# Optimization experiments

Measured on AMD Instinct MI355X. Metric: run time of the kernel, lower is better.

## Reference

```python
import jax, jax.numpy as jnp
import numpy as np

B, NQ, NK = 8, 1024, 1024
DQ = DK = DV = 512
H = 8
DS = DV // H
EPS = 1e-4
MAX_ITER = 3
SQRT_V = DV ** 0.25  # sqrt(sqrt(dim_V))


def setup_inputs() -> dict:
    key = jax.random.key(0)
    ks = jax.random.split(key, 8)
    s = 0.02
    return {
        "Q": jax.random.normal(ks[0], (B, NQ, DQ), jnp.float32),
        "K": jax.random.normal(ks[1], (B, NK, DK), jnp.float32),
        "Wq": jax.random.normal(ks[2], (DV, DQ), jnp.float32) * s,
        "bq": jnp.zeros((DV,), jnp.float32),
        "Wk": jax.random.normal(ks[3], (DV, DK), jnp.float32) * s,
        "bk": jnp.zeros((DV,), jnp.float32),
        "Wv": jax.random.normal(ks[4], (DV, DK), jnp.float32) * s,
        "bv": jnp.zeros((DV,), jnp.float32),
        "Wo": jax.random.normal(ks[5], (DV, DV), jnp.float32) * s,
        "bo": jnp.zeros((DV,), jnp.float32),
    }


def _split_heads(x):
    # torch.cat(x.split(ds, 2), 0): head-major stacking along batch
    b, n, _ = x.shape
    return x.reshape(b, n, H, DS).transpose(2, 0, 1, 3).reshape(H * b, n, DS)


def _merge_heads(x, b):
    # torch.cat(x.split(b, 0), 2): inverse of _split_heads
    _, n, ds = x.shape
    return x.reshape(H, b, n, ds).transpose(1, 2, 0, 3).reshape(b, n, H * ds)


def _sinkhorn_plan(x, y):
    # x: [M, P1, d], y: [M, P2, d]; cost = pairwise Euclidean (p=2) distance.
    x2 = jnp.sum(x * x, axis=-1)[:, :, None]
    y2 = jnp.sum(y * y, axis=-1)[:, None, :]
    C = jnp.sqrt(jnp.maximum(x2 + y2 - 2.0 * jnp.einsum("mid,mjd->mij", x, y), 0.0))
    m, p1, p2 = C.shape
    log_a = -jnp.log(jnp.float32(p1))  # uniform marginals
    log_b = -jnp.log(jnp.float32(p2))
    u = jnp.zeros((m, p1), C.dtype)
    v = jnp.zeros((m, p2), C.dtype)
    for _ in range(MAX_ITER):  # fixed small iteration count (max_iter=3)
        u = EPS * (log_a - jax.scipy.special.logsumexp((v[:, None, :] - C) / EPS, axis=2))
        v = EPS * (log_b - jax.scipy.special.logsumexp((u[:, :, None] - C) / EPS, axis=1))
    # transport plan P: [M, P1, P2]
    return jnp.exp((u[:, :, None] + v[:, None, :] - C) / EPS)


def reference(Q, K, Wq, bq, Wk, bk, Wv, bv, Wo, bo):
    q = Q @ Wq.T + bq            # [B, NQ, DV]
    k = K @ Wk.T + bk            # [B, NK, DV]
    v = K @ Wv.T + bv            # [B, NK, DV]
    b = Q.shape[0]
    q_, k_, v_ = _split_heads(q), _split_heads(k), _split_heads(v)  # [H*B, N, DS]
    A = _sinkhorn_plan(q_ / SQRT_V, k_ / SQRT_V)                    # [H*B, NQ, NK]
    O = _merge_heads(q_ + jnp.einsum("mij,mjd->mid", A, v_), b)     # [B, NQ, DV]
    return O + jax.nn.relu(O @ Wo.T + bo)
```

## Files before the change

kernel.cpp:

```cpp
#include <hip/hip_runtime.h>
#include <hip/hip_bf16.h>
#include <math.h>

#define NB 8
#define NN 1024
#define ND 512
#define NH 8
#define NDS 64
#define NM 64
#define LOG_A (-6.93147180559945f)
#define SQRT_V 4.75682846001088f
#define INV_SQRT_V 0.210224103813429f
#define INV_EPS 10000.0f
#define L2E  1.44269504088896f
#define LN2F 0.693147180559945f
#define IEL2 14426.9504088896f

#define SPLIT_ELEMS ((size_t)NM * NN * NDS)
#define W_ELEMS     ((size_t)ND * ND)
#define UV_FLOATS   ((size_t)NM * NN)

typedef unsigned short u16;
typedef unsigned int   u32;
typedef __attribute__((ext_vector_type(8))) short bf16x8;
typedef __attribute__((ext_vector_type(4))) float f32x4;

#define MFMA16(a,b,c) __builtin_amdgcn_mfma_f32_16x16x32_bf16(a,b,c,0,0,0)

__device__ __forceinline__ u16 f2bf_t(float x) {
  return (u16)(__float_as_uint(x) >> 16);
}
__device__ __forceinline__ float bf2f(u16 h) {
  return __uint_as_float(((u32)h) << 16);
}
__device__ __forceinline__ float fast_sqrt(float x) {
  float r;
  asm("v_sqrt_f32 %0, %1" : "=v"(r) : "v"(x));
  return r;
}
__device__ __forceinline__ float fast_exp2(float x) {
  float r;
  asm("v_exp_f32 %0, %1" : "=v"(r) : "v"(x));
  return r;
}
__device__ __forceinline__ float max3f(float a, float b, float c) {
  float r;
  asm("v_max3_f32 %0, %1, %2, %3" : "=v"(r) : "v"(a), "v"(b), "v"(c));
  return r;
}
__device__ __forceinline__ void soft_barrier() {
  asm volatile("s_waitcnt lgkmcnt(0)" ::: "memory");
  __builtin_amdgcn_sched_barrier(0);
  __builtin_amdgcn_s_barrier();
  __builtin_amdgcn_sched_barrier(0);
  asm volatile("" ::: "memory");
}

__global__ __launch_bounds__(256) void k_split(
    const float* __restrict__ X, u16* __restrict__ hi, u16* __restrict__ lo)
{
  const size_t i = ((size_t)blockIdx.x * 256 + threadIdx.x) * 4;
  float4 v = *(const float4*)&X[i];
  const float* vp = (const float*)&v;
  u16 h[4], l[4];
#pragma unroll
  for (int j = 0; j < 4; ++j) {
    h[j] = f2bf_t(vp[j]);
    l[j] = f2bf_t(vp[j] - bf2f(h[j]));
  }
  uint2 ph, pl;
  ph.x = (u32)h[0] | ((u32)h[1] << 16);
  ph.y = (u32)h[2] | ((u32)h[3] << 16);
  pl.x = (u32)l[0] | ((u32)l[1] << 16);
  pl.y = (u32)l[2] | ((u32)l[3] << 16);
  *(uint2*)&hi[i] = ph;
  *(uint2*)&lo[i] = pl;
}

__global__ __launch_bounds__(256, 2) void k_proj_mfma(
    const u16* __restrict__ Xh, const u16* __restrict__ Xl,
    const u16* __restrict__ Wh, const u16* __restrict__ Wl,
    const float* __restrict__ bias, u16* __restrict__ oh,
    u16* __restrict__ ol, u16* __restrict__ oT,
    float* __restrict__ nrm, float scale, int mode)
{
  __shared__ __align__(16) u16 Xhs[2][64][72];
  __shared__ __align__(16) u16 Xls[2][64][72];
  __shared__ __align__(16) u16 Whs[2][64][72];
  __shared__ __align__(16) u16 Wls[2][64][72];
  const int t = threadIdx.x;
  const int r0 = blockIdx.x * 64;
  const int h  = blockIdx.y;
  const int c0 = h * 64;
  const int w = t >> 6, l = t & 63;
  const int c = l & 15, kg = l >> 4;
  const int srow = t >> 2;
  const int skoff = (t & 3) * 16;

  const u16* gxh = &Xh[(size_t)(r0 + srow) * ND + skoff];
  const u16* gxl = &Xl[(size_t)(r0 + srow) * ND + skoff];
  const u16* gwh = &Wh[(size_t)(c0 + srow) * ND + skoff];
  const u16* gwl = &Wl[(size_t)(c0 + srow) * ND + skoff];

  bf16x8 rxh0 = *(const bf16x8*)gxh, rxh1 = *(const bf16x8*)(gxh + 8);
  bf16x8 rxl0 = *(const bf16x8*)gxl, rxl1 = *(const bf16x8*)(gxl + 8);
  bf16x8 rwh0 = *(const bf16x8*)gwh, rwh1 = *(const bf16x8*)(gwh + 8);
  bf16x8 rwl0 = *(const bf16x8*)gwl, rwl1 = *(const bf16x8*)(gwl + 8);

  f32x4 acc[4];
#pragma unroll
  for (int cf = 0; cf < 4; ++cf) acc[cf] = (f32x4){0.f, 0.f, 0.f, 0.f};

  for (int kt = 0; kt < 8; ++kt) {
    const int buf = kt & 1;
    *(bf16x8*)&Xhs[buf][srow][skoff]     = rxh0;
    *(bf16x8*)&Xhs[buf][srow][skoff + 8] = rxh1;
    *(bf16x8*)&Xls[buf][srow][skoff]     = rxl0;
    *(bf16x8*)&Xls[buf][srow][skoff + 8] = rxl1;
    *(bf16x8*)&Whs[buf][srow][skoff]     = rwh0;
    *(bf16x8*)&Whs[buf][srow][skoff + 8] = rwh1;
    *(bf16x8*)&Wls[buf][srow][skoff]     = rwl0;
    *(bf16x8*)&Wls[buf][srow][skoff + 8] = rwl1;
    {
      const int nk = ((kt + 1) & 7) * 64;
      rxh0 = *(const bf16x8*)(gxh + nk); rxh1 = *(const bf16x8*)(gxh + nk + 8);
      rxl0 = *(const bf16x8*)(gxl + nk); rxl1 = *(const bf16x8*)(gxl + nk + 8);
      rwh0 = *(const bf16x8*)(gwh + nk); rwh1 = *(const bf16x8*)(gwh + nk + 8);
      rwl0 = *(const bf16x8*)(gwl + nk); rwl1 = *(const bf16x8*)(gwl + nk + 8);
    }
    soft_barrier();
#pragma unroll
    for (int ks = 0; ks < 2; ++ks) {
      bf16x8 Ah = *(const bf16x8*)&Xhs[buf][w * 16 + c][ks * 32 + kg * 8];
      bf16x8 Al = *(const bf16x8*)&Xls[buf][w * 16 + c][ks * 32 + kg * 8];
#pragma unroll
      for (int cf = 0; cf < 4; ++cf) {
        bf16x8 Bh = *(const bf16x8*)&Whs[buf][cf * 16 + c][ks * 32 + kg * 8];
        bf16x8 Bl = *(const bf16x8*)&Wls[buf][cf * 16 + c][ks * 32 + kg * 8];
        acc[cf] = MFMA16(Ah, Bh, acc[cf]);
        acc[cf] = MFMA16(Ah, Bl, acc[cf]);
        acc[cf] = MFMA16(Al, Bh, acc[cf]);
      }
    }
  }

  const int bb = r0 >> 10;
  const int n0 = r0 & 1023;
  const size_t mrow = (size_t)(h * NB + bb) * NN;
  if (mode == 0) {
    float ns[4] = {0.f, 0.f, 0.f, 0.f};
#pragma unroll
    for (int cf = 0; cf < 4; ++cf) {
      const int col = c0 + cf * 16 + c;
      const float bv = bias[col];
#pragma unroll
      for (int r = 0; r < 4; ++r) {
        float v = (acc[cf][r] + bv) * scale;
        u16 hv = f2bf_t(v);
        u16 lv = f2bf_t(v - bf2f(hv));
        ns[r] = fmaf(v, v, ns[r]);
        int n = n0 + w * 16 + kg * 4 + r;
        size_t idx = (mrow + n) * NDS + cf * 16 + c;
        oh[idx] = hv;
        ol[idx] = lv;
      }
    }
#pragma unroll
    for (int off = 1; off <= 8; off <<= 1)
#pragma unroll
      for (int r = 0; r < 4; ++r) ns[r] += __shfl_xor(ns[r], off);
    if (c == 0) {
#pragma unroll
      for (int r = 0; r < 4; ++r)
        nrm[mrow + n0 + w * 16 + kg * 4 + r] = ns[r];
    }
  } else {
#pragma unroll
    for (int cf = 0; cf < 4; ++cf) {
      const int d = cf * 16 + c;
      const float bv = bias[c0 + d];
      u16 p0 = f2bf_t((acc[cf][0] + bv) * scale);
      u16 p1 = f2bf_t((acc[cf][1] + bv) * scale);
      u16 p2 = f2bf_t((acc[cf][2] + bv) * scale);
      u16 p3 = f2bf_t((acc[cf][3] + bv) * scale);
      uint2 p;
      p.x = (u32)p0 | ((u32)p1 << 16);
      p.y = (u32)p2 | ((u32)p3 << 16);
      *(uint2*)&oT[((size_t)(h * NB + bb) * NDS + d) * NN + n0 + w * 16 + kg * 4] = p;
    }
  }
}

__global__ __launch_bounds__(512, 4) void k_lse_mfma(
    const u16* __restrict__ Ah_, const u16* __restrict__ Bh_,
    const float* __restrict__ Anrm, const float* __restrict__ Bnrm,
    const float* __restrict__ din, float* __restrict__ dout, int first)
{
  __shared__ __align__(16) float din_s[NN];
  __shared__ __align__(16) float y2_s[NN];
  __shared__ __align__(16) u16 Bhs[2][64][72];
  const int t = threadIdx.x;
  const int Lb = blockIdx.x;
  const int xcd = Lb & 7, slot = Lb >> 3;
  const int m = xcd + 8 * (slot >> 3);
  const int a0 = (slot & 7) * 128;

  if (first) {
    *(float2*)&din_s[t * 2] = make_float2(0.f, 0.f);
  } else {
    float2 dv = *(const float2*)&din[(size_t)m * NN + t * 2];
    dv.x *= L2E; dv.y *= L2E;
    *(float2*)&din_s[t * 2] = dv;
  }
  *(float2*)&y2_s[t * 2] = *(const float2*)&Bnrm[(size_t)m * NN + t * 2];

  const int w = t >> 6, l = t & 63;
  const int c = l & 15, kg = l >> 4;
  const int arow = a0 + w * 16;
  const size_t mbase = (size_t)m * NN * NDS;

  const u16* pah = &Ah_[mbase + (size_t)(arow + c) * NDS + kg * 8];
  bf16x8 A0h = *(const bf16x8*)pah;
  bf16x8 A1h = *(const bf16x8*)(pah + 32);

  float x2r[4];
#pragma unroll
  for (int r = 0; r < 4; ++r) x2r[r] = Anrm[(size_t)m * NN + arow + kg * 4 + r];
  float M[4], S[4];
#pragma unroll
  for (int r = 0; r < 4; ++r) { M[r] = -3.0e38f; S[r] = 0.f; }

  const int srow = t >> 3;
  const int skoff = (t & 7) * 8;
  const u16* gh = &Bh_[mbase + (size_t)srow * NDS + skoff];
  bf16x8 rh = *(const bf16x8*)gh;
  __syncthreads();

  for (int bt = 0; bt < 16; ++bt) {
    const int b0 = bt * 64;
    const int buf = bt & 1;
    *(bf16x8*)&Bhs[buf][srow][skoff] = rh;
    {
      const size_t noff = (size_t)((bt + 1) & 15) * 4096;
      rh = *(const bf16x8*)(gh + noff);
    }
    soft_barrier();
    f32x4 acc[4];
#pragma unroll
    for (int cf = 0; cf < 4; ++cf) {
      const int bl = cf * 16 + c;
      bf16x8 B0h = *(const bf16x8*)&Bhs[buf][bl][kg * 8];
      bf16x8 B1h = *(const bf16x8*)&Bhs[buf][bl][kg * 8 + 32];
      f32x4 a = {0.f, 0.f, 0.f, 0.f};
      a = MFMA16(A0h, B0h, a);
      a = MFMA16(A1h, B1h, a);
      acc[cf] = a;
    }
    float X[4][4];
#pragma unroll
    for (int cf = 0; cf < 4; ++cf) {
      const int col = b0 + cf * 16 + c;
      const float vb2 = din_s[col];
      const float y2  = y2_s[col];
#pragma unroll
      for (int r = 0; r < 4; ++r) {
        float d2 = fmaf(-2.f, acc[cf][r], x2r[r] + y2);
        float sq = fast_sqrt(fmaxf(d2, 0.f));
        X[cf][r] = fmaf(-IEL2, sq, vb2);
      }
    }
#pragma unroll
    for (int r = 0; r < 4; ++r) {
      float m1 = max3f(X[0][r], X[1][r], X[2][r]);
      float nm = max3f(m1, X[3][r], M[r]);
      float s4 = fast_exp2(X[0][r] - nm) + fast_exp2(X[1][r] - nm)
               + fast_exp2(X[2][r] - nm) + fast_exp2(X[3][r] - nm);
      S[r] = fmaf(S[r], fast_exp2(M[r] - nm), s4);
      M[r] = nm;
    }
  }
#pragma unroll
  for (int off = 1; off <= 8; off <<= 1) {
#pragma unroll
    for (int r = 0; r < 4; ++r) {
      float Mo = __shfl_xor(M[r], off);
      float So = __shfl_xor(S[r], off);
      float nm = fmaxf(M[r], Mo);
      S[r] = S[r] * fast_exp2(M[r] - nm) + So * fast_exp2(Mo - nm);
      M[r] = nm;
    }
  }
  if (c == 0) {
#pragma unroll
    for (int r = 0; r < 4; ++r)
      dout[(size_t)m * NN + arow + kg * 4 + r] =
          LOG_A - M[r] * LN2F - __logf(S[r]);
  }
}

__global__ __launch_bounds__(512, 4) void k_pv_mfma(
    const u16* __restrict__ qh, const u16* __restrict__ ql,
    const u16* __restrict__ kh, const u16* __restrict__ vT,
    const float* __restrict__ qn, const float* __restrict__ kn,
    const float* __restrict__ ue, const float* __restrict__ ve,
    u16* __restrict__ Oh_, u16* __restrict__ Ol_)
{
  __shared__ __align__(16) float ve_s[NN];
  __shared__ __align__(16) float y2_s[NN];
  __shared__ __align__(16) u16 Bhs[2][64][72];
  __shared__ __align__(16) u16 Vs[2][64][72];
  __shared__ __align__(16) u16 pT[8][16][40];
  const int t = threadIdx.x;
  const int Lb = blockIdx.x;
  const int xcd = Lb & 7, slot = Lb >> 3;
  const int m = xcd + 8 * (slot >> 3);
  const int a0 = (slot & 7) * 128;
  {
    float2 vv = *(const float2*)&ve[(size_t)m * NN + t * 2];
    vv.x *= L2E; vv.y *= L2E;
    *(float2*)&ve_s[t * 2] = vv;
  }
  *(float2*)&y2_s[t * 2] = *(const float2*)&kn[(size_t)m * NN + t * 2];

  const int w = t >> 6, l = t & 63;
  const int c = l & 15, kg = l >> 4;
  const int arow = a0 + w * 16;
  const size_t mbase = (size_t)m * NN * NDS;

  const u16* pah = &qh[mbase + (size_t)(arow + c) * NDS + kg * 8];
  bf16x8 A0h = *(const bf16x8*)pah;
  bf16x8 A1h = *(const bf16x8*)(pah + 32);

  float x2r[4], uer2[4];
#pragma unroll
  for (int r = 0; r < 4; ++r) {
    x2r[r]  = qn[(size_t)m * NN + arow + kg * 4 + r];
    uer2[r] = ue[(size_t)m * NN + arow + kg * 4 + r] * L2E;
  }
  f32x4 pacc[4];
#pragma unroll
  for (int df = 0; df < 4; ++df) pacc[df] = (f32x4){0.f, 0.f, 0.f, 0.f};

  const int srow = t >> 3;
  const int skoff = (t & 7) * 8;
  const u16* gh = &kh[mbase + (size_t)srow * NDS + skoff];
  const u16* gv = &vT[((size_t)m * NDS + srow) * NN + skoff];
  bf16x8 rh = *(const bf16x8*)gh;
  bf16x8 rv = *(const bf16x8*)gv;
  __syncthreads();

  for (int bt = 0; bt < 16; ++bt) {
    const int b0 = bt * 64;
    const int buf = bt & 1;
    *(bf16x8*)&Bhs[buf][srow][skoff] = rh;
    *(bf16x8*)&Vs[buf][srow][skoff]  = rv;
    {
      const int nbt = (bt + 1) & 15;
      rh = *(const bf16x8*)(gh + (size_t)nbt * 4096);
      rv = *(const bf16x8*)(gv + (size_t)nbt * 64);
    }
    soft_barrier();
#pragma unroll
    for (int ph = 0; ph < 2; ++ph) {
      f32x4 acc[2];
#pragma unroll
      for (int q = 0; q < 2; ++q) {
        const int cf = ph * 2 + q;
        const int bl = cf * 16 + c;
        bf16x8 B0h = *(const bf16x8*)&Bhs[buf][bl][kg * 8];
        bf16x8 B1h = *(const bf16x8*)&Bhs[buf][bl][kg * 8 + 32];
        f32x4 a = {0.f, 0.f, 0.f, 0.f};
        a = MFMA16(A0h, B0h, a);
        a = MFMA16(A1h, B1h, a);
        acc[q] = a;
      }
#pragma unroll
      for (int q = 0; q < 2; ++q) {
        const int cf = ph * 2 + q;
        const int col = b0 + cf * 16 + c;
        const float ve2 = ve_s[col];
        const float y2  = y2_s[col];
#pragma unroll
        for (int r = 0; r < 4; ++r) {
          float d2 = fmaf(-2.f, acc[q][r], x2r[r] + y2);
          float sq = fast_sqrt(fmaxf(d2, 0.f));
          float p  = fast_exp2(fmaf(-IEL2, sq, uer2[r] + ve2));
          pT[w][kg * 4 + r][q * 16 + c] = f2bf_t(p);
        }
      }
      bf16x8 Pa = *(const bf16x8*)&pT[w][c][kg * 8];
#pragma unroll
      for (int df = 0; df < 4; ++df) {
        bf16x8 Vb = *(const bf16x8*)&Vs[buf][df * 16 + c][ph * 32 + kg * 8];
        pacc[df] = MFMA16(Pa, Vb, pacc[df]);
      }
    }
  }
#pragma unroll
  for (int df = 0; df < 4; ++df) {
#pragma unroll
    for (int r = 0; r < 4; ++r) {
      int row = arow + kg * 4 + r;
      int d = df * 16 + c;
      size_t qi = mbase + (size_t)row * NDS + d;
      float qv = bf2f(qh[qi]) + bf2f(ql[qi]);
      float o  = fmaf(SQRT_V, qv, pacc[df][r]);
      u16 hv = f2bf_t(o);
      Oh_[qi] = hv;
      Ol_[qi] = f2bf_t(o - bf2f(hv));
    }
  }
}

__global__ __launch_bounds__(256, 2) void k_out_mfma(
    const u16* __restrict__ Oh_, const u16* __restrict__ Ol_,
    const u16* __restrict__ Wh, const u16* __restrict__ Wl,
    const float* __restrict__ bo, float* __restrict__ out)
{
  __shared__ __align__(16) u16 Ahs[2][64][72];
  __shared__ __align__(16) u16 Als[2][64][72];
  __shared__ __align__(16) u16 Whs[2][64][72];
  __shared__ __align__(16) u16 Wls[2][64][72];
  const int t = threadIdx.x;
  const int r0 = blockIdx.x * 64;
  const int c0 = blockIdx.y * 64;
  const int bb = r0 >> 10;
  const int n0 = r0 & 1023;
  const int w = t >> 6, l = t & 63;
  const int c = l & 15, kg = l >> 4;
  const int srow = t >> 2;
  const int skoff = (t & 3) * 16;

  f32x4 acc[4];
#pragma unroll
  for (int cf = 0; cf < 4; ++cf) acc[cf] = (f32x4){0.f, 0.f, 0.f, 0.f};

  bf16x8 rah0, rah1, ral0, ral1, rwh0, rwh1, rwl0, rwl1;
  {
    const size_t ob = ((size_t)(0 * NB + bb) * NN + n0 + srow) * NDS;
    const u16* gah = &Oh_[ob + skoff];
    const u16* gal = &Ol_[ob + skoff];
    const u16* gwh = &Wh[(size_t)(c0 + srow) * ND + skoff];
    const u16* gwl = &Wl[(size_t)(c0 + srow) * ND + skoff];
    rah0 = *(const bf16x8*)gah; rah1 = *(const bf16x8*)(gah + 8);
    ral0 = *(const bf16x8*)gal; ral1 = *(const bf16x8*)(gal + 8);
    rwh0 = *(const bf16x8*)gwh; rwh1 = *(const bf16x8*)(gwh + 8);
    rwl0 = *(const bf16x8*)gwl; rwl1 = *(const bf16x8*)(gwl + 8);
  }

  for (int kt = 0; kt < 8; ++kt) {
    const int buf = kt & 1;
    *(bf16x8*)&Ahs[buf][srow][skoff]     = rah0;
    *(bf16x8*)&Ahs[buf][srow][skoff + 8] = rah1;
    *(bf16x8*)&Als[buf][srow][skoff]     = ral0;
    *(bf16x8*)&Als[buf][srow][skoff + 8] = ral1;
    *(bf16x8*)&Whs[buf][srow][skoff]     = rwh0;
    *(bf16x8*)&Whs[buf][srow][skoff + 8] = rwh1;
    *(bf16x8*)&Wls[buf][srow][skoff]     = rwl0;
    *(bf16x8*)&Wls[buf][srow][skoff + 8] = rwl1;
    {
      const int nkt = (kt + 1) & 7;
      const size_t ob = ((size_t)(nkt * NB + bb) * NN + n0 + srow) * NDS;
      const u16* gah = &Oh_[ob + skoff];
      const u16* gal = &Ol_[ob + skoff];
      const u16* gwh = &Wh[(size_t)(c0 + srow) * ND + nkt * 64 + skoff];
      const u16* gwl = &Wl[(size_t)(c0 + srow) * ND + nkt * 64 + skoff];
      rah0 = *(const bf16x8*)gah; rah1 = *(const bf16x8*)(gah + 8);
      ral0 = *(const bf16x8*)gal; ral1 = *(const bf16x8*)(gal + 8);
      rwh0 = *(const bf16x8*)gwh; rwh1 = *(const bf16x8*)(gwh + 8);
      rwl0 = *(const bf16x8*)gwl; rwl1 = *(const bf16x8*)(gwl + 8);
    }
    soft_barrier();
#pragma unroll
    for (int ks = 0; ks < 2; ++ks) {
      bf16x8 Ah = *(const bf16x8*)&Ahs[buf][w * 16 + c][ks * 32 + kg * 8];
      bf16x8 Al = *(const bf16x8*)&Als[buf][w * 16 + c][ks * 32 + kg * 8];
#pragma unroll
      for (int cf = 0; cf < 4; ++cf) {
        bf16x8 Bh = *(const bf16x8*)&Whs[buf][cf * 16 + c][ks * 32 + kg * 8];
        bf16x8 Bl = *(const bf16x8*)&Wls[buf][cf * 16 + c][ks * 32 + kg * 8];
        acc[cf] = MFMA16(Ah, Bh, acc[cf]);
        acc[cf] = MFMA16(Ah, Bl, acc[cf]);
        acc[cf] = MFMA16(Al, Bh, acc[cf]);
      }
    }
  }
#pragma unroll
  for (int cf = 0; cf < 4; ++cf) {
    const int col = c0 + cf * 16 + c;
    const int d = cf * 16 + c;
    const float bv = bo[col];
#pragma unroll
    for (int r = 0; r < 4; ++r) {
      const int n = n0 + w * 16 + kg * 4 + r;
      const size_t oi = ((size_t)(blockIdx.y * NB + bb) * NN + n) * NDS + d;
      float om = bf2f(Oh_[oi]) + bf2f(Ol_[oi]);
      out[(size_t)(r0 + w * 16 + kg * 4 + r) * ND + col] =
          om + fmaxf(acc[cf][r] + bv, 0.f);
    }
  }
}

extern "C" void kernel_launch(void* const* d_in, const int* in_sizes, int n_in,
                              void* d_out, int out_size, void* d_ws, size_t ws_size,
                              hipStream_t stream) {
  const float* Q  = (const float*)d_in[0];
  const float* K  = (const float*)d_in[1];
  const float* Wq = (const float*)d_in[2];
  const float* bq = (const float*)d_in[3];
  const float* Wk = (const float*)d_in[4];
  const float* bk = (const float*)d_in[5];
  const float* Wv = (const float*)d_in[6];
  const float* bv = (const float*)d_in[7];
  const float* Wo = (const float*)d_in[8];
  const float* bo = (const float*)d_in[9];
  float* out = (float*)d_out;

  const size_t need_bytes =
      7 * SPLIT_ELEMS * sizeof(u16) + 8 * W_ELEMS * sizeof(u16) +
      4 * UV_FLOATS * sizeof(float);
  if (ws_size < need_bytes) return;

  u16* qh = (u16*)d_ws;
  u16* ql = qh + SPLIT_ELEMS;
  u16* kh = ql + SPLIT_ELEMS;
  u16* kl = kh + SPLIT_ELEMS;
  u16* vT = kl + SPLIT_ELEMS;
  u16* Oh = vT + SPLIT_ELEMS;
  u16* Ol = Oh + SPLIT_ELEMS;
  u16* wqh = Ol + SPLIT_ELEMS;
  u16* wql = wqh + W_ELEMS;
  u16* wkh = wql + W_ELEMS;
  u16* wkl = wkh + W_ELEMS;
  u16* wvh = wkl + W_ELEMS;
  u16* wvl = wvh + W_ELEMS;
  u16* woh = wvl + W_ELEMS;
  u16* wol = woh + W_ELEMS;
  float* ue = (float*)(wol + W_ELEMS);
  float* ve = ue + UV_FLOATS;
  float* qn = ve + UV_FLOATS;
  float* kn = qn + UV_FLOATS;

  u16* Qrh = Oh;
  u16* Qrl = Ol;
  u16* Krh = (u16*)d_out;
  u16* Krl = Krh + SPLIT_ELEMS;

  dim3 blk(256);
  k_split<<<dim3(4096), blk, 0, stream>>>(Q, Qrh, Qrl);
  k_split<<<dim3(4096), blk, 0, stream>>>(K, Krh, Krl);
  k_split<<<dim3(256), blk, 0, stream>>>(Wq, wqh, wql);
  k_split<<<dim3(256), blk, 0, stream>>>(Wk, wkh, wkl);
  k_split<<<dim3(256), blk, 0, stream>>>(Wv, wvh, wvl);
  k_split<<<dim3(256), blk, 0, stream>>>(Wo, woh, wol);
  k_proj_mfma<<<dim3(128, 8), blk, 0, stream>>>(Qrh, Qrl, wqh, wql, bq, qh, ql, nullptr, qn, INV_SQRT_V, 0);
  k_proj_mfma<<<dim3(128, 8), blk, 0, stream>>>(Krh, Krl, wkh, wkl, bk, kh, kl, nullptr, kn, INV_SQRT_V, 0);
  k_proj_mfma<<<dim3(128, 8), blk, 0, stream>>>(Krh, Krl, wvh, wvl, bv, nullptr, nullptr, vT, nullptr, 1.0f, 1);
  for (int it = 0; it < 3; ++it) {
    k_lse_mfma<<<dim3(512), dim3(512), 0, stream>>>(qh, kh, qn, kn, ve, ue, it == 0 ? 1 : 0);
    k_lse_mfma<<<dim3(512), dim3(512), 0, stream>>>(kh, qh, kn, qn, ue, ve, 0);
  }
  k_pv_mfma<<<dim3(512), dim3(512), 0, stream>>>(qh, ql, kh, vT, qn, kn, ue, ve, Oh, Ol);
  k_out_mfma<<<dim3(128, 8), blk, 0, stream>>>(Oh, Ol, woh, wol, bo, out);
}
```

Measured before the change: 311.1 us.

## Fuse input bf16 split into projections and skip negligible exp terms

Result: slower. 329.4 us (+5.9%).

```diff
diff --git a/kernel.cpp b/kernel.cpp
--- a/kernel.cpp
+++ b/kernel.cpp
@@ -15,6 +15,7 @@
 #define L2E  1.44269504088896f
 #define LN2F 0.693147180559945f
 #define IEL2 14426.9504088896f
+#define SKIP_THR 30.0f
 
 #define SPLIT_ELEMS ((size_t)NM * NN * NDS)
 #define W_ELEMS     ((size_t)ND * ND)
@@ -54,6 +55,18 @@
   __builtin_amdgcn_s_barrier();
   __builtin_amdgcn_sched_barrier(0);
   asm volatile("" ::: "memory");
+}
+__device__ __forceinline__ void split_pack8(float4 a, float4 b,
+                                            bf16x8& ho, bf16x8& lo_) {
+  float f[8] = {a.x, a.y, a.z, a.w, b.x, b.y, b.z, b.w};
+  union { u16 u[8]; bf16x8 v; } H, L;
+#pragma unroll
+  for (int j = 0; j < 8; ++j) {
+    u16 hv = f2bf_t(f[j]);
+    H.u[j] = hv;
+    L.u[j] = f2bf_t(f[j] - bf2f(hv));
+  }
+  ho = H.v; lo_ = L.v;
 }
 
 __global__ __launch_bounds__(256) void k_split(
@@ -78,7 +91,7 @@
 }
 
 __global__ __launch_bounds__(256, 2) void k_proj_mfma(
-    const u16* __restrict__ Xh, const u16* __restrict__ Xl,
+    const float* __restrict__ Xf,
     const u16* __restrict__ Wh, const u16* __restrict__ Wl,
     const float* __restrict__ bias, u16* __restrict__ oh,
     u16* __restrict__ ol, u16* __restrict__ oT,
@@ -97,13 +110,14 @@
   const int srow = t >> 2;
   const int skoff = (t & 3) * 16;
 
-  const u16* gxh = &Xh[(size_t)(r0 + srow) * ND + skoff];
-  const u16* gxl = &Xl[(size_t)(r0 + srow) * ND + skoff];
+  const float* gx = &Xf[(size_t)(r0 + srow) * ND + skoff];
   const u16* gwh = &Wh[(size_t)(c0 + srow) * ND + skoff];
   const u16* gwl = &Wl[(size_t)(c0 + srow) * ND + skoff];
 
-  bf16x8 rxh0 = *(const bf16x8*)gxh, rxh1 = *(const bf16x8*)(gxh + 8);
-  bf16x8 rxl0 = *(const bf16x8*)gxl, rxl1 = *(const bf16x8*)(gxl + 8);
+  float4 fx0 = *(const float4*)gx;
+  float4 fx1 = *(const float4*)(gx + 4);
+  float4 fx2 = *(const float4*)(gx + 8);
+  float4 fx3 = *(const float4*)(gx + 12);
   bf16x8 rwh0 = *(const bf16x8*)gwh, rwh1 = *(const bf16x8*)(gwh + 8);
   bf16x8 rwl0 = *(const bf16x8*)gwl, rwl1 = *(const bf16x8*)(gwl + 8);
 
@@ -113,18 +127,25 @@
 
   for (int kt = 0; kt < 8; ++kt) {
     const int buf = kt & 1;
-    *(bf16x8*)&Xhs[buf][srow][skoff]     = rxh0;
-    *(bf16x8*)&Xhs[buf][srow][skoff + 8] = rxh1;
-    *(bf16x8*)&Xls[buf][srow][skoff]     = rxl0;
-    *(bf16x8*)&Xls[buf][srow][skoff + 8] = rxl1;
+    {
+      bf16x8 h0, l0, h1, l1;
+      split_pack8(fx0, fx1, h0, l0);
+      split_pack8(fx2, fx3, h1, l1);
+      *(bf16x8*)&Xhs[buf][srow][skoff]     = h0;
+      *(bf16x8*)&Xhs[buf][srow][skoff + 8] = h1;
+      *(bf16x8*)&Xls[buf][srow][skoff]     = l0;
+      *(bf16x8*)&Xls[buf][srow][skoff + 8] = l1;
+    }
     *(bf16x8*)&Whs[buf][srow][skoff]     = rwh0;
     *(bf16x8*)&Whs[buf][srow][skoff + 8] = rwh1;
     *(bf16x8*)&Wls[buf][srow][skoff]     = rwl0;
     *(bf16x8*)&Wls[buf][srow][skoff + 8] = rwl1;
     {
       const int nk = ((kt + 1) & 7) * 64;
-      rxh0 = *(const bf16x8*)(gxh + nk); rxh1 = *(const bf16x8*)(gxh + nk + 8);
-      rxl0 = *(const bf16x8*)(gxl + nk); rxl1 = *(const bf16x8*)(gxl + nk + 8);
+      fx0 = *(const float4*)(gx + nk);
+      fx1 = *(const float4*)(gx + nk + 4);
+      fx2 = *(const float4*)(gx + nk + 8);
+      fx3 = *(const float4*)(gx + nk + 12);
       rwh0 = *(const bf16x8*)(gwh + nk); rwh1 = *(const bf16x8*)(gwh + nk + 8);
       rwl0 = *(const bf16x8*)(gwl + nk); rwl1 = *(const bf16x8*)(gwl + nk + 8);
     }
@@ -272,11 +293,14 @@
 #pragma unroll
     for (int r = 0; r < 4; ++r) {
       float m1 = max3f(X[0][r], X[1][r], X[2][r]);
-      float nm = max3f(m1, X[3][r], M[r]);
-      float s4 = fast_exp2(X[0][r] - nm) + fast_exp2(X[1][r] - nm)
-               + fast_exp2(X[2][r] - nm) + fast_exp2(X[3][r] - nm);
-      S[r] = fmaf(S[r], fast_exp2(M[r] - nm), s4);
-      M[r] = nm;
+      float xm = fmaxf(m1, X[3][r]);
+      if (__any(xm > M[r] - SKIP_THR)) {
+        float nm = fmaxf(xm, M[r]);
+        float s4 = fast_exp2(X[0][r] - nm) + fast_exp2(X[1][r] - nm)
+                 + fast_exp2(X[2][r] - nm) + fast_exp2(X[3][r] - nm);
+        S[r] = fmaf(S[r], fast_exp2(M[r] - nm), s4);
+        M[r] = nm;
+      }
     }
   }
 #pragma unroll
@@ -380,12 +404,22 @@
         const int col = b0 + cf * 16 + c;
         const float ve2 = ve_s[col];
         const float y2  = y2_s[col];
+        float arg[4];
 #pragma unroll
         for (int r = 0; r < 4; ++r) {
           float d2 = fmaf(-2.f, acc[q][r], x2r[r] + y2);
           float sq = fast_sqrt(fmaxf(d2, 0.f));
-          float p  = fast_exp2(fmaf(-IEL2, sq, uer2[r] + ve2));
-          pT[w][kg * 4 + r][q * 16 + c] = f2bf_t(p);
+          arg[r] = fmaf(-IEL2, sq, uer2[r] + ve2);
+        }
+        float am = fmaxf(max3f(arg[0], arg[1], arg[2]), arg[3]);
+        if (__any(am > -SKIP_THR)) {
+#pragma unroll
+          for (int r = 0; r < 4; ++r)
+            pT[w][kg * 4 + r][q * 16 + c] = f2bf_t(fast_exp2(arg[r]));
+        } else {
+#pragma unroll
+          for (int r = 0; r < 4; ++r)
+            pT[w][kg * 4 + r][q * 16 + c] = 0;
         }
       }
       bf16x8 Pa = *(const bf16x8*)&pT[w][c][kg * 8];
@@ -541,21 +575,14 @@
   float* qn = ve + UV_FLOATS;
   float* kn = qn + UV_FLOATS;
 
-  u16* Qrh = Oh;
-  u16* Qrl = Ol;
-  u16* Krh = (u16*)d_out;
-  u16* Krl = Krh + SPLIT_ELEMS;
-
   dim3 blk(256);
-  k_split<<<dim3(4096), blk, 0, stream>>>(Q, Qrh, Qrl);
-  k_split<<<dim3(4096), blk, 0, stream>>>(K, Krh, Krl);
   k_split<<<dim3(256), blk, 0, stream>>>(Wq, wqh, wql);
   k_split<<<dim3(256), blk, 0, stream>>>(Wk, wkh, wkl);
   k_split<<<dim3(256), blk, 0, stream>>>(Wv, wvh, wvl);
   k_split<<<dim3(256), blk, 0, stream>>>(Wo, woh, wol);
-  k_proj_mfma<<<dim3(128, 8), blk, 0, stream>>>(Qrh, Qrl, wqh, wql, bq, qh, ql, nullptr, qn, INV_SQRT_V, 0);
-  k_proj_mfma<<<dim3(128, 8), blk, 0, stream>>>(Krh, Krl, wkh, wkl, bk, kh, kl, nullptr, kn, INV_SQRT_V, 0);
-  k_proj_mfma<<<dim3(128, 8), blk, 0, stream>>>(Krh, Krl, wvh, wvl, bv, nullptr, nullptr, vT, nullptr, 1.0f, 1);
+  k_proj_mfma<<<dim3(128, 8), blk, 0, stream>>>(Q, wqh, wql, bq, qh, ql, nullptr, qn, INV_SQRT_V, 0);
+  k_proj_mfma<<<dim3(128, 8), blk, 0, stream>>>(K, wkh, wkl, bk, kh, kl, nullptr, kn, INV_SQRT_V, 0);
+  k_proj_mfma<<<dim3(128, 8), blk, 0, stream>>>(K, wvh, wvl, bv, nullptr, nullptr, vT, nullptr, 1.0f, 1);
   for (int it = 0; it < 3; ++it) {
     k_lse_mfma<<<dim3(512), dim3(512), 0, stream>>>(qh, kh, qn, kn, ve, ue, it == 0 ? 1 : 0);
     k_lse_mfma<<<dim3(512), dim3(512), 0, stream>>>(kh, qh, kn, qn, ue, ve, 0);
```
